# Performance work log

Measured on AMD Instinct MI355X. Metric: run time of the kernel, lower is better.

## Reference

```python
import jax, jax.numpy as jnp
import numpy as np

N = 100000      # nodes
E = 1600000     # random edges (self-loops appended, as PyG GATConv does)
IN = 128        # in_channels
HID = 8         # hidden_channels per head
HEADS = 8
OUT = 40        # out_channels (classes)
NEG_SLOPE = 0.2 # PyG GATConv default


def _xavier(k, shape, fan_in, fan_out):
    lim = np.sqrt(6.0 / (fan_in + fan_out)).astype(np.float32)
    return jax.random.uniform(k, shape, jnp.float32, -lim, lim)


def setup_inputs() -> dict:
    key = jax.random.key(0)
    ks = jax.random.split(key, 8)
    x = jax.random.normal(ks[0], (N, IN), jnp.float32)
    ei = jax.random.randint(ks[1], (2, E), 0, N)
    loops = jnp.arange(N)
    edge_index = jnp.concatenate([ei, jnp.stack([loops, loops])], axis=1)  # [2, E+N]
    W1 = _xavier(ks[2], (HEADS * HID, IN), IN, HEADS * HID)
    att_src1 = _xavier(ks[3], (HEADS, HID), HID, 1)
    att_dst1 = _xavier(ks[4], (HEADS, HID), HID, 1)
    b1 = jnp.zeros((HEADS * HID,), jnp.float32)
    W2 = _xavier(ks[5], (OUT, HEADS * HID), HEADS * HID, OUT)
    att_src2 = _xavier(ks[6], (1, OUT), OUT, 1)
    att_dst2 = _xavier(ks[7], (1, OUT), OUT, 1)
    b2 = jnp.zeros((OUT,), jnp.float32)
    return {"x": x, "edge_index": edge_index, "W1": W1, "att_src1": att_src1,
            "att_dst1": att_dst1, "b1": b1, "W2": W2, "att_src2": att_src2,
            "att_dst2": att_dst2, "b2": b2}


def _gat_conv(x, src, dst, W, a_src, a_dst, b, heads, ch, concat):
    n = x.shape[0]
    h = (x @ W.T).reshape(n, heads, ch)                       # [N,H,C]
    a_s = jnp.sum(h * a_src[None], axis=-1)                   # [N,H]
    a_d = jnp.sum(h * a_dst[None], axis=-1)                   # [N,H]
    e = jax.nn.leaky_relu(a_s[src] + a_d[dst], NEG_SLOPE)     # [Eall,H]
    # segment softmax over edges sharing a destination node
    e_max = jax.ops.segment_max(e, dst, num_segments=n)
    ex = jnp.exp(e - e_max[dst])
    denom = jax.ops.segment_sum(ex, dst, num_segments=n)
    alpha = ex / denom[dst]                                   # [Eall,H]
    msg = h[src] * alpha[:, :, None]                          # [Eall,H,C]
    out = jax.ops.segment_sum(msg, dst, num_segments=n)       # [N,H,C]
    out = out.reshape(n, heads * ch) if concat else out.mean(axis=1)
    return out + b


def reference(x, edge_index, W1, att_src1, att_dst1, b1, W2, att_src2, att_dst2, b2):
    # eval mode: dropout is identity
    src, dst = edge_index[0], edge_index[1]
    h = _gat_conv(x, src, dst, W1, att_src1, att_dst1, b1, HEADS, HID, True)
    h = jax.nn.elu(h)
    out = _gat_conv(h, src, dst, W2, att_src2, att_dst2, b2, 1, OUT, False)
    return out
```

## Files before the change

### kernel.cpp

```cpp
#include <hip/hip_runtime.h>
#include <hip/hip_bf16.h>

#define IN_CH   128
#define HID     8
#define HEADS   8
#define C1      64
#define OUT_CH  40
#define NEG     0.2f
#define NPART   8

typedef __attribute__((ext_vector_type(8))) short  short8;
typedef __attribute__((ext_vector_type(4))) float  f32x4;

__device__ __forceinline__ float b2f(unsigned short u) {
    return __uint_as_float(((unsigned int)u) << 16);
}
__device__ __forceinline__ float blo(unsigned int p) { return __uint_as_float(p << 16); }
__device__ __forceinline__ float bhi(unsigned int p) { return __uint_as_float(p & 0xffff0000u); }
__device__ __forceinline__ unsigned short f2b(float f) {
    unsigned int u = __float_as_uint(f);
    unsigned int r = (u + 0x7fffu + ((u >> 16) & 1u)) >> 16;
    return (unsigned short)r;
}
__device__ __forceinline__ float lrelu(float v) { return v > 0.f ? v : NEG * v; }

#define P_W1    0
#define P_AS1   8192
#define P_AD1   8256
#define P_B1    8320
#define P_W2    8384
#define P_AS2   10944
#define P_AD2   10984
#define P_B2    11024
#define P_TOT   11064

__global__ __launch_bounds__(256) void kA_fused(
        const unsigned int* __restrict__ x32,
        const void* W1, const void* as1p, const void* ad1p, const void* b1,
        const void* W2, const void* as2p, const void* ad2p, const void* b2,
        const int* __restrict__ dst, int* __restrict__ deg,
        int* __restrict__ flag, float* __restrict__ pf,
        unsigned short* __restrict__ w1bf,
        int e_all, int n_nodes) {
    int t = threadIdx.x;
    __shared__ int sflag;
    if (t < 64) {
        unsigned int lo = x32[t] & 0xffffu;
        int ex = (int)((lo >> 7) & 0xff);
        bool sane = (ex >= 112 && ex <= 143);
        unsigned long long m = __ballot(sane);
        if (t == 0) {
            int isbf = (__popcll(m) >= 32) ? 1 : 0;
            sflag = isbf;
            if (blockIdx.x == 0) *flag = isbf;
        }
    }
    __syncthreads();
    const int isbf = sflag;

    if (blockIdx.x < 8) {
        int g = blockIdx.x * 256 + t;
#define CONV(dstoff, srcp, cnt)                                         \
        if (isbf) {                                                     \
            const unsigned short* sp = (const unsigned short*)(srcp);   \
            for (int i = g; i < (cnt); i += 2048) pf[(dstoff) + i] = b2f(sp[i]); \
        } else {                                                        \
            const float* sp = (const float*)(srcp);                     \
            for (int i = g; i < (cnt); i += 2048) pf[(dstoff) + i] = sp[i]; \
        }
        CONV(P_W1,  W1, 8192)
        CONV(P_AS1, as1p, 64)
        CONV(P_AD1, ad1p, 64)
        CONV(P_B1,  b1, 64)
        CONV(P_W2,  W2, 2560)
        CONV(P_AS2, as2p, 40)
        CONV(P_AD2, ad2p, 40)
        CONV(P_B2,  b2, 40)
#undef CONV
        if (isbf) {
            const unsigned short* sp = (const unsigned short*)W1;
            for (int i = g; i < 8192; i += 2048) w1bf[i] = sp[i];
        } else {
            const float* sp = (const float*)W1;
            for (int i = g; i < 8192; i += 2048) w1bf[i] = f2b(sp[i]);
        }
    }

    int part = blockIdx.x & (NPART - 1);
    int nm   = gridDim.x >> 3;
    int mblk = blockIdx.x >> 3;
    int lo = (int)((long long)part * n_nodes / NPART);
    int hi = (int)((long long)(part + 1) * n_nodes / NPART);
    const int4* dst4 = (const int4*)dst;
    int e4n = e_all >> 2;
    for (int i = mblk * 256 + t; i < e4n; i += nm * 256) {
        int4 d4 = dst4[i];
        if (d4.x >= lo && d4.x < hi) atomicAdd(&deg[d4.x], 1);
        if (d4.y >= lo && d4.y < hi) atomicAdd(&deg[d4.y], 1);
        if (d4.z >= lo && d4.z < hi) atomicAdd(&deg[d4.z], 1);
        if (d4.w >= lo && d4.w < hi) atomicAdd(&deg[d4.w], 1);
    }
    for (int e = (e4n << 2) + mblk * 256 + t; e < e_all; e += nm * 256) {
        int d = dst[e];
        if (d >= lo && d < hi) atomicAdd(&deg[d], 1);
    }
}

__global__ __launch_bounds__(256) void kB1_scan(
        const int* __restrict__ deg, int* __restrict__ offs,
        int* __restrict__ bsum, int n) {
    __shared__ int sd[256];
    int t = threadIdx.x;
    int i = blockIdx.x * 256 + t;
    int v = (i < n) ? deg[i] : 0;
    sd[t] = v;
    __syncthreads();
    for (int off = 1; off < 256; off <<= 1) {
        int u = (t >= off) ? sd[t - off] : 0;
        __syncthreads();
        sd[t] += u;
        __syncthreads();
    }
    if (i < n) offs[i] = sd[t] - v;
    if (t == 255) bsum[blockIdx.x] = sd[255];
}

__global__ __launch_bounds__(512) void kB2_scanb(
        const int* __restrict__ bsum, int* __restrict__ bsumx, int nb) {
    __shared__ int sd[512];
    int t = threadIdx.x;
    int v = (t < nb) ? bsum[t] : 0;
    sd[t] = v;
    __syncthreads();
    for (int off = 1; off < 512; off <<= 1) {
        int u = (t >= off) ? sd[t - off] : 0;
        __syncthreads();
        sd[t] += u;
        __syncthreads();
    }
    if (t < nb) bsumx[t] = sd[t] - v;
}

__global__ __launch_bounds__(256) void kB3_fix(
        int* __restrict__ offs, const int* __restrict__ bsumx,
        int* __restrict__ cursor, int n) {
    int i = blockIdx.x * 256 + threadIdx.x;
    if (i >= n) return;
    int o = offs[i] + bsumx[blockIdx.x];
    offs[i] = o;
    cursor[i] = o;
}

__global__ __launch_bounds__(256) void kC_scatter(
        const int* __restrict__ src, const int* __restrict__ dst,
        int* __restrict__ cursor, int* __restrict__ csr_src,
        int e_all, int n_nodes) {
    int part = blockIdx.x & (NPART - 1);
    int nm   = gridDim.x >> 3;
    int mblk = blockIdx.x >> 3;
    int lo = (int)((long long)part * n_nodes / NPART);
    int hi = (int)((long long)(part + 1) * n_nodes / NPART);
    const int4* dst4 = (const int4*)dst;
    int e4n = e_all >> 2;
    for (int i = mblk * 256 + threadIdx.x; i < e4n; i += nm * 256) {
        int4 d4 = dst4[i];
        int eb = i << 2;
        if (d4.x >= lo && d4.x < hi) { int p = atomicAdd(&cursor[d4.x], 1); csr_src[p] = src[eb]; }
        if (d4.y >= lo && d4.y < hi) { int p = atomicAdd(&cursor[d4.y], 1); csr_src[p] = src[eb + 1]; }
        if (d4.z >= lo && d4.z < hi) { int p = atomicAdd(&cursor[d4.z], 1); csr_src[p] = src[eb + 2]; }
        if (d4.w >= lo && d4.w < hi) { int p = atomicAdd(&cursor[d4.w], 1); csr_src[p] = src[eb + 3]; }
    }
    for (int e = (e4n << 2) + mblk * 256 + threadIdx.x; e < e_all; e += nm * 256) {
        int d = dst[e];
        if (d >= lo && d < hi) { int p = atomicAdd(&cursor[d], 1); csr_src[p] = src[e]; }
    }
}

__global__ __launch_bounds__(256) void k1_mfma(
        const void* __restrict__ x, const unsigned short* __restrict__ w1bf,
        const float* __restrict__ pf, const int* __restrict__ flagp,
        unsigned short* __restrict__ h1b, float* __restrict__ as1, float* __restrict__ ad1,
        int n_nodes) {
    int tid = threadIdx.x;
    int wv = tid >> 6, L = tid & 63;
    int m = L & 15, q = L >> 4;
    int base = blockIdx.x * 64 + wv * 16;
    if (base >= n_nodes) return;
    const int isbf = *flagp;

    short8 bfr[4][4];
#pragma unroll
    for (int t = 0; t < 4; ++t)
#pragma unroll
        for (int kb = 0; kb < 4; ++kb)
            bfr[t][kb] = *(const short8*)(w1bf + (size_t)(t * 16 + m) * IN_CH + kb * 32 + q * 8);

    int row = base + m;
    if (row >= n_nodes) row = n_nodes - 1;
    short8 af[4];
    if (isbf) {
        const unsigned short* xr = (const unsigned short*)x + (size_t)row * IN_CH + q * 8;
#pragma unroll
        for (int kb = 0; kb < 4; ++kb) af[kb] = *(const short8*)(xr + kb * 32);
    } else {
        const float* xr = (const float*)x + (size_t)row * IN_CH + q * 8;
#pragma unroll
        for (int kb = 0; kb < 4; ++kb) {
            short8 a;
#pragma unroll
            for (int j = 0; j < 8; ++j) a[j] = (short)f2b(xr[kb * 32 + j]);
            af[kb] = a;
        }
    }

    f32x4 acc[4];
#pragma unroll
    for (int t = 0; t < 4; ++t) acc[t] = (f32x4){0.f, 0.f, 0.f, 0.f};
#pragma unroll
    for (int t = 0; t < 4; ++t)
#pragma unroll
        for (int kb = 0; kb < 4; ++kb)
            acc[t] = __builtin_amdgcn_mfma_f32_16x16x32_bf16(af[kb], bfr[t][kb], acc[t], 0, 0, 0);

#pragma unroll
    for (int t = 0; t < 4; ++t) {
#pragma unroll
        for (int r = 0; r < 4; ++r) {
            int node = base + q * 4 + r;
            bool ok = (node < n_nodes);
            float val = acc[t][r];
            int ch = t * 16 + m;
            if (ok) h1b[(size_t)node * C1 + ch] = f2b(val);
            float ps = val * pf[P_AS1 + ch];
            float pd = val * pf[P_AD1 + ch];
            ps += __shfl_xor(ps, 1, 64); ps += __shfl_xor(ps, 2, 64); ps += __shfl_xor(ps, 4, 64);
            pd += __shfl_xor(pd, 1, 64); pd += __shfl_xor(pd, 2, 64); pd += __shfl_xor(pd, 4, 64);
            if (ok && (L & 7) == 0) {
                int head = 2 * t + ((m >> 3) & 1);
                as1[(size_t)node * HEADS + head] = ps;
                ad1[(size_t)node * HEADS + head] = pd;
            }
        }
    }
}

__global__ __launch_bounds__(256) void k34_fused(
        const int* __restrict__ offs, const int* __restrict__ deg,
        const int* __restrict__ csr_src,
        const float* __restrict__ as1, const float* __restrict__ ad1,
        const unsigned short* __restrict__ h1b, const float* __restrict__ pf,
        unsigned short* __restrict__ h2b, float* __restrict__ as2v, float* __restrict__ ad2v,
        int n_nodes) {
    int tid = threadIdx.x;
    int w = tid >> 6, t = tid & 63;
    __shared__ float wTf[4096];
    __shared__ float xsf[4 * C1];
    for (int e = tid; e < 2560; e += 256) {
        int row = e >> 6, k = e & 63;
        int g = k >> 2, j = k & 3;
        wTf[(g * 64 + ((row + g) & 63)) * 4 + j] = pf[P_W2 + e];
    }
    __syncthreads();
    int d = blockIdx.x * 4 + w;
    if (d >= n_nodes) return;

    int head = t >> 3;
    int j8 = t >> 3, h8 = t & 7;
    float adv1 = ad1[(size_t)d * HEADS + h8];
    int start = offs[d];
    int dg = deg[d];
    float acc = 0.f, den = 0.f;
    int nfull = dg & ~7;
    int base = 0;
    for (; base < nfull; base += 8) {
        int s = csr_src[start + base + j8];
        float v = as1[(size_t)s * HEADS + h8] + adv1;
        float wgt = __expf(lrelu(v));
#pragma unroll
        for (int jj = 0; jj < 8; ++jj) {
            int sj   = __shfl(s, jj * 8, 64);
            float wj = __shfl(wgt, jj * 8 + head, 64);
            float hv = b2f(h1b[(size_t)sj * C1 + t]);
            den += wj;
            acc += wj * hv;
        }
    }
    int rem = dg - nfull;
    if (rem) {
        int s = 0; float wgt = 0.f;
        if (j8 < rem) {
            s = csr_src[start + base + j8];
            float v = as1[(size_t)s * HEADS + h8] + adv1;
            wgt = __expf(lrelu(v));
        }
        for (int jj = 0; jj < rem; ++jj) {
            int sj   = __shfl(s, jj * 8, 64);
            float wj = __shfl(wgt, jj * 8 + head, 64);
            float hv = b2f(h1b[(size_t)sj * C1 + t]);
            den += wj;
            acc += wj * hv;
        }
    }
    float o = acc / den + pf[P_B1 + t];
    o = o > 0.f ? o : (__expf(o) - 1.f);
    xsf[w * C1 + t] = o;

    const float4* wT4 = (const float4*)wTf;
    float hs = 0.f, hd = 0.f;
    if (t < OUT_CH) {
        const float4* xv = (const float4*)(xsf + w * C1);
        float a2 = 0.f;
#pragma unroll
        for (int g = 0; g < 16; ++g) {
            float4 wv = wT4[g * 64 + ((t + g) & 63)];
            float4 x4 = xv[g];
            a2 += x4.x * wv.x + x4.y * wv.y + x4.z * wv.z + x4.w * wv.w;
        }
        h2b[(size_t)d * OUT_CH + t] = f2b(a2);
        hs = a2 * pf[P_AS2 + t];
        hd = a2 * pf[P_AD2 + t];
    }
    for (int off = 1; off < 64; off <<= 1) {
        hs += __shfl_xor(hs, off, 64);
        hd += __shfl_xor(hd, off, 64);
    }
    if (t == 0) { as2v[d] = hs; ad2v[d] = hd; }
}

__global__ __launch_bounds__(256) void k6_fused2(
        const int* __restrict__ offs, const int* __restrict__ deg,
        const int* __restrict__ csr_src,
        const float* __restrict__ as2, const float* __restrict__ ad2,
        const unsigned short* __restrict__ h2b, const float* __restrict__ pf,
        const int* __restrict__ flagp, void* __restrict__ outp, int n_nodes) {
    int d = blockIdx.x * 4 + (threadIdx.x >> 6);
    if (d >= n_nodes) return;
    int t = threadIdx.x & 63;
    float adv = ad2[d];
    int start = offs[d];
    int dg = deg[d];
    bool act = (t < OUT_CH);
    int tc = act ? t : 0;
    float acc = 0.f, den = 0.f;
    int nfull = dg & ~15;
    int base = 0;
    for (; base < nfull; base += 16) {
        int s = 0; float w = 0.f;
        if (t < 16) {
            s = csr_src[start + base + t];
            w = __expf(lrelu(as2[s] + adv));
        }
#pragma unroll
        for (int jj = 0; jj < 16; ++jj) {
            int sj   = __shfl(s, jj, 64);
            float wj = __shfl(w, jj, 64);
            float hv = b2f(h2b[(size_t)sj * OUT_CH + tc]);
            den += wj;
            acc += wj * hv;
        }
    }
    int rem = dg - nfull;
    if (rem) {
        int s = 0; float w = 0.f;
        if (t < rem) {
            s = csr_src[start + base + t];
            w = __expf(lrelu(as2[s] + adv));
        }
        for (int jj = 0; jj < rem; ++jj) {
            int sj   = __shfl(s, jj, 64);
            float wj = __shfl(w, jj, 64);
            float hv = b2f(h2b[(size_t)sj * OUT_CH + tc]);
            den += wj;
            acc += wj * hv;
        }
    }
    if (!act) return;
    float o = acc / den + pf[P_B2 + t];
    size_t idx = (size_t)d * OUT_CH + t;
    if (*flagp) ((unsigned short*)outp)[idx] = f2b(o);
    else        ((float*)outp)[idx] = o;
}

extern "C" void kernel_launch(void* const* d_in, const int* in_sizes, int n_in,
                              void* d_out, int out_size, void* d_ws, size_t ws_size,
                              hipStream_t stream) {
    const void* x  = d_in[0];
    const int*  ei = (const int*)d_in[1];

    const int n_nodes = in_sizes[0] / IN_CH;
    const int e_all   = in_sizes[1] / 2;
    const int* srcI = ei;
    const int* dstI = ei + e_all;

    float* ws = (float*)d_ws;
    const size_t n = (size_t)n_nodes;
    int* deg     = (int*)ws;
    int* offs    = deg + n;
    int* cursor  = offs + n;
    int* bsum    = cursor + n;
    int* bsumx   = bsum + 512;
    int* csr_src = bsumx + 512;
    float* A     = ws + 3 * n + 1024 + (size_t)e_all;
    float* as1   = A;
    float* ad1   = A + 8 * n;
    unsigned short* h1b = (unsigned short*)(A + 16 * n);
    float* as2   = A + 48 * n;
    float* ad2   = A + 49 * n;
    unsigned short* h2b = (unsigned short*)(A + 50 * n);
    int*   flagp = (int*)(A + 70 * n);
    float* pf    = A + 70 * n + 16;
    unsigned short* w1bf = (unsigned short*)(pf + P_TOT);

    hipMemsetAsync(deg, 0, n * sizeof(int), stream);

    kA_fused<<<1024, 256, 0, stream>>>((const unsigned int*)x,
        d_in[2], d_in[3], d_in[4], d_in[5], d_in[6], d_in[7], d_in[8], d_in[9],
        dstI, deg, flagp, pf, w1bf, e_all, n_nodes);

    int nb = (n_nodes + 255) / 256;
    kB1_scan<<<nb, 256, 0, stream>>>(deg, offs, bsum, n_nodes);
    kB2_scanb<<<1, 512, 0, stream>>>(bsum, bsumx, nb);
    kB3_fix<<<nb, 256, 0, stream>>>(offs, bsumx, cursor, n_nodes);

    kC_scatter<<<1024, 256, 0, stream>>>(srcI, dstI, cursor, csr_src, e_all, n_nodes);

    k1_mfma<<<(n_nodes + 63) / 64, 256, 0, stream>>>(x, w1bf, pf, flagp, h1b, as1, ad1, n_nodes);

    k34_fused<<<(n_nodes + 3) / 4, 256, 0, stream>>>(offs, deg, csr_src, as1, ad1, h1b, pf, h2b, as2, ad2, n_nodes);

    k6_fused2<<<(n_nodes + 3) / 4, 256, 0, stream>>>(offs, deg, csr_src, as2, ad2, h2b, pf, flagp, d_out, n_nodes);
}
```

Baseline: 466.0 us.

## Split layer-1 aggregation from GEMM2 and use atomic single-pass CSR offset allocation

The fused aggregation+GEMM2 kernel is split in two. The aggregation kernel now writes the ELU output as bf16 to a new buffer. A separate GEMM2 kernel handles 32 nodes per block, so each block stages the 10KB W2 transpose in shared memory once for 32 nodes instead of once per 4 nodes. This also frees that shared memory from the aggregation kernel, which may raise its occupancy. The three-kernel prefix scan becomes one kernel in which each block reserves its offset range with a global atomic. That removes two launches, but block ranges land in nondeterministic order, and the bf16 round-trip of the intermediate adds rounding error and extra global traffic.

```diff
diff --git a/kernel.cpp b/kernel.cpp
--- a/kernel.cpp
+++ b/kernel.cpp
@@ -106,10 +106,11 @@
     }
 }
 
-__global__ __launch_bounds__(256) void kB1_scan(
+__global__ __launch_bounds__(256) void kB_alloc(
         const int* __restrict__ deg, int* __restrict__ offs,
-        int* __restrict__ bsum, int n) {
+        int* __restrict__ cursor, int* __restrict__ counter, int n) {
     __shared__ int sd[256];
+    __shared__ int sbase;
     int t = threadIdx.x;
     int i = blockIdx.x * 256 + t;
     int v = (i < n) ? deg[i] : 0;
@@ -121,34 +122,13 @@
         sd[t] += u;
         __syncthreads();
     }
-    if (i < n) offs[i] = sd[t] - v;
-    if (t == 255) bsum[blockIdx.x] = sd[255];
-}
-
-__global__ __launch_bounds__(512) void kB2_scanb(
-        const int* __restrict__ bsum, int* __restrict__ bsumx, int nb) {
-    __shared__ int sd[512];
-    int t = threadIdx.x;
-    int v = (t < nb) ? bsum[t] : 0;
-    sd[t] = v;
+    if (t == 255) sbase = atomicAdd(counter, sd[255]);
     __syncthreads();
-    for (int off = 1; off < 512; off <<= 1) {
-        int u = (t >= off) ? sd[t - off] : 0;
-        __syncthreads();
-        sd[t] += u;
-        __syncthreads();
-    }
-    if (t < nb) bsumx[t] = sd[t] - v;
-}
-
-__global__ __launch_bounds__(256) void kB3_fix(
-        int* __restrict__ offs, const int* __restrict__ bsumx,
-        int* __restrict__ cursor, int n) {
-    int i = blockIdx.x * 256 + threadIdx.x;
-    if (i >= n) return;
-    int o = offs[i] + bsumx[blockIdx.x];
-    offs[i] = o;
-    cursor[i] = o;
+    if (i < n) {
+        int o = sbase + sd[t] - v;
+        offs[i] = o;
+        cursor[i] = o;
+    }
 }
 
 __global__ __launch_bounds__(256) void kC_scatter(
@@ -244,26 +224,15 @@
     }
 }
 
-__global__ __launch_bounds__(256) void k34_fused(
+__global__ __launch_bounds__(256) void k3_fused1(
         const int* __restrict__ offs, const int* __restrict__ deg,
         const int* __restrict__ csr_src,
         const float* __restrict__ as1, const float* __restrict__ ad1,
         const unsigned short* __restrict__ h1b, const float* __restrict__ pf,
-        unsigned short* __restrict__ h2b, float* __restrict__ as2v, float* __restrict__ ad2v,
-        int n_nodes) {
-    int tid = threadIdx.x;
-    int w = tid >> 6, t = tid & 63;
-    __shared__ float wTf[4096];
-    __shared__ float xsf[4 * C1];
-    for (int e = tid; e < 2560; e += 256) {
-        int row = e >> 6, k = e & 63;
-        int g = k >> 2, j = k & 3;
-        wTf[(g * 64 + ((row + g) & 63)) * 4 + j] = pf[P_W2 + e];
-    }
-    __syncthreads();
-    int d = blockIdx.x * 4 + w;
+        unsigned short* __restrict__ x2, int n_nodes) {
+    int d = blockIdx.x * 4 + (threadIdx.x >> 6);
     if (d >= n_nodes) return;
-
+    int t = threadIdx.x & 63;
     int head = t >> 3;
     int j8 = t >> 3, h8 = t & 7;
     float adv1 = ad1[(size_t)d * HEADS + h8];
@@ -275,11 +244,11 @@
     for (; base < nfull; base += 8) {
         int s = csr_src[start + base + j8];
         float v = as1[(size_t)s * HEADS + h8] + adv1;
-        float wgt = __expf(lrelu(v));
+        float w = __expf(lrelu(v));
 #pragma unroll
         for (int jj = 0; jj < 8; ++jj) {
             int sj   = __shfl(s, jj * 8, 64);
-            float wj = __shfl(wgt, jj * 8 + head, 64);
+            float wj = __shfl(w, jj * 8 + head, 64);
             float hv = b2f(h1b[(size_t)sj * C1 + t]);
             den += wj;
             acc += wj * hv;
@@ -287,15 +256,15 @@
     }
     int rem = dg - nfull;
     if (rem) {
-        int s = 0; float wgt = 0.f;
+        int s = 0; float w = 0.f;
         if (j8 < rem) {
             s = csr_src[start + base + j8];
             float v = as1[(size_t)s * HEADS + h8] + adv1;
-            wgt = __expf(lrelu(v));
+            w = __expf(lrelu(v));
         }
         for (int jj = 0; jj < rem; ++jj) {
             int sj   = __shfl(s, jj * 8, 64);
-            float wj = __shfl(wgt, jj * 8 + head, 64);
+            float wj = __shfl(w, jj * 8 + head, 64);
             float hv = b2f(h1b[(size_t)sj * C1 + t]);
             den += wj;
             acc += wj * hv;
@@ -303,28 +272,57 @@
     }
     float o = acc / den + pf[P_B1 + t];
     o = o > 0.f ? o : (__expf(o) - 1.f);
-    xsf[w * C1 + t] = o;
-
+    x2[(size_t)d * C1 + t] = f2b(o);
+}
+
+__global__ __launch_bounds__(256) void k4_gemm2(
+        const unsigned short* __restrict__ x2, const float* __restrict__ pf,
+        unsigned short* __restrict__ h2b, float* __restrict__ as2, float* __restrict__ ad2,
+        int n_nodes) {
+    int tid = threadIdx.x;
+    int w = tid >> 6, t = tid & 63;
+    __shared__ float wTf[4096];
+    __shared__ float xsf[4 * C1];
+    for (int e = tid; e < 2560; e += 256) {
+        int row = e >> 6, k = e & 63;
+        int g = k >> 2, j = k & 3;
+        wTf[(g * 64 + ((row + g) & 63)) * 4 + j] = pf[P_W2 + e];
+    }
+    __syncthreads();
     const float4* wT4 = (const float4*)wTf;
-    float hs = 0.f, hd = 0.f;
-    if (t < OUT_CH) {
-        const float4* xv = (const float4*)(xsf + w * C1);
-        float a2 = 0.f;
-#pragma unroll
-        for (int g = 0; g < 16; ++g) {
-            float4 wv = wT4[g * 64 + ((t + g) & 63)];
-            float4 x4 = xv[g];
-            a2 += x4.x * wv.x + x4.y * wv.y + x4.z * wv.z + x4.w * wv.w;
-        }
-        h2b[(size_t)d * OUT_CH + t] = f2b(a2);
-        hs = a2 * pf[P_AS2 + t];
-        hd = a2 * pf[P_AD2 + t];
-    }
-    for (int off = 1; off < 64; off <<= 1) {
-        hs += __shfl_xor(hs, off, 64);
-        hd += __shfl_xor(hd, off, 64);
-    }
-    if (t == 0) { as2v[d] = hs; ad2v[d] = hd; }
+    int base = blockIdx.x * 32 + w * 8;
+    for (int i = 0; i < 8; ++i) {
+        int n = base + i;
+        bool ok = (n < n_nodes);
+        if (ok && t < 32) {
+            unsigned int p = ((const unsigned int*)x2)[(size_t)n * 32 + t];
+            xsf[w * C1 + 2 * t]     = blo(p);
+            xsf[w * C1 + 2 * t + 1] = bhi(p);
+        }
+        __syncthreads();
+        if (ok) {
+            float hs = 0.f, hd = 0.f;
+            if (t < OUT_CH) {
+                const float4* xv = (const float4*)(xsf + w * C1);
+                float acc = 0.f;
+#pragma unroll
+                for (int g = 0; g < 16; ++g) {
+                    float4 wv = wT4[g * 64 + ((t + g) & 63)];
+                    float4 x4 = xv[g];
+                    acc += x4.x * wv.x + x4.y * wv.y + x4.z * wv.z + x4.w * wv.w;
+                }
+                h2b[(size_t)n * OUT_CH + t] = f2b(acc);
+                hs = acc * pf[P_AS2 + t];
+                hd = acc * pf[P_AD2 + t];
+            }
+            for (int off = 1; off < 64; off <<= 1) {
+                hs += __shfl_xor(hs, off, 64);
+                hd += __shfl_xor(hd, off, 64);
+            }
+            if (t == 0) { as2[n] = hs; ad2[n] = hd; }
+        }
+        __syncthreads();
+    }
 }
 
 __global__ __launch_bounds__(256) void k6_fused2(
@@ -395,38 +393,38 @@
     float* ws = (float*)d_ws;
     const size_t n = (size_t)n_nodes;
     int* deg     = (int*)ws;
-    int* offs    = deg + n;
-    int* cursor  = offs + n;
-    int* bsum    = cursor + n;
-    int* bsumx   = bsum + 512;
-    int* csr_src = bsumx + 512;
-    float* A     = ws + 3 * n + 1024 + (size_t)e_all;
+    int* counter = deg + n;
+    int* offs    = (int*)(ws + n + 16);
+    int* cursor  = (int*)(ws + 2 * n + 16);
+    int* csr_src = (int*)(ws + 3 * n + 32);
+    float* A     = ws + 3 * n + 32 + (size_t)e_all;
     float* as1   = A;
     float* ad1   = A + 8 * n;
     unsigned short* h1b = (unsigned short*)(A + 16 * n);
-    float* as2   = A + 48 * n;
-    float* ad2   = A + 49 * n;
-    unsigned short* h2b = (unsigned short*)(A + 50 * n);
-    int*   flagp = (int*)(A + 70 * n);
-    float* pf    = A + 70 * n + 16;
+    unsigned short* x2  = (unsigned short*)(A + 48 * n);
+    float* as2   = A + 80 * n;
+    float* ad2   = A + 81 * n;
+    unsigned short* h2b = (unsigned short*)(A + 82 * n);
+    int*   flagp = (int*)(A + 102 * n);
+    float* pf    = A + 102 * n + 16;
     unsigned short* w1bf = (unsigned short*)(pf + P_TOT);
 
-    hipMemsetAsync(deg, 0, n * sizeof(int), stream);
+    hipMemsetAsync(ws, 0, (n + 16) * sizeof(int), stream);
 
     kA_fused<<<1024, 256, 0, stream>>>((const unsigned int*)x,
         d_in[2], d_in[3], d_in[4], d_in[5], d_in[6], d_in[7], d_in[8], d_in[9],
         dstI, deg, flagp, pf, w1bf, e_all, n_nodes);
 
     int nb = (n_nodes + 255) / 256;
-    kB1_scan<<<nb, 256, 0, stream>>>(deg, offs, bsum, n_nodes);
-    kB2_scanb<<<1, 512, 0, stream>>>(bsum, bsumx, nb);
-    kB3_fix<<<nb, 256, 0, stream>>>(offs, bsumx, cursor, n_nodes);
+    kB_alloc<<<nb, 256, 0, stream>>>(deg, offs, cursor, counter, n_nodes);
 
     kC_scatter<<<1024, 256, 0, stream>>>(srcI, dstI, cursor, csr_src, e_all, n_nodes);
 
     k1_mfma<<<(n_nodes + 63) / 64, 256, 0, stream>>>(x, w1bf, pf, flagp, h1b, as1, ad1, n_nodes);
 
-    k34_fused<<<(n_nodes + 3) / 4, 256, 0, stream>>>(offs, deg, csr_src, as1, ad1, h1b, pf, h2b, as2, ad2, n_nodes);
+    k3_fused1<<<(n_nodes + 3) / 4, 256, 0, stream>>>(offs, deg, csr_src, as1, ad1, h1b, pf, x2, n_nodes);
+
+    k4_gemm2<<<(n_nodes + 31) / 32, 256, 0, stream>>>(x2, pf, h2b, as2, ad2, n_nodes);
 
     k6_fused2<<<(n_nodes + 3) / 4, 256, 0, stream>>>(offs, deg, csr_src, as2, ad2, h2b, pf, flagp, d_out, n_nodes);
 }
```

Result: no change. 464.2 us (-0.4%).
